# Kernel optimization log

Measured on AMD Instinct MI355X. Metric: run time of the kernel, lower is better.

The kernel has to match this reference:

```python
import jax, jax.numpy as jnp
import numpy as np

BATCH = 4096
DIM = 256
TEMP = 0.5
COS_EPS = 1e-8  # torch.nn.CosineSimilarity default eps


def setup_inputs() -> dict:
    key = jax.random.key(0)
    k1, k2 = jax.random.split(key)
    zis = jax.random.normal(k1, (BATCH, DIM), dtype=jnp.float32)
    zjs = jax.random.normal(k2, (BATCH, DIM), dtype=jnp.float32)
    return {"zis": zis, "zjs": zjs}


def reference(zis, zjs):
    n = zis.shape[0]  # batch_size
    # representations = cat([zjs, zis]) -> (2N, D)
    reps = jnp.concatenate([zjs, zis], axis=0)
    # cosine similarity matrix: dot / max(|x||y|, eps)  (matches torch CosineSimilarity)
    norms = jnp.linalg.norm(reps, axis=-1)  # (2N,)
    sim = (reps @ reps.T) / jnp.maximum(norms[:, None] * norms[None, :], COS_EPS)  # (2N, 2N)
    # positives: diag at offset +N (rows 0..N-1) then offset -N (rows N..2N-1)
    pos = jnp.concatenate([jnp.diagonal(sim, n), jnp.diagonal(sim, -n)])  # (2N,)
    # CE with label 0 over [pos, negatives]: negatives = row minus {diag, positive};
    # logsumexp([pos] + negatives) == logsumexp(row with only the self-diagonal masked),
    # since the positive appears exactly once in the row.
    two_n = 2 * n
    logits = sim / TEMP
    logits = jnp.where(jnp.eye(two_n, dtype=bool), -jnp.inf, logits)
    lse = jax.nn.logsumexp(logits, axis=-1)  # (2N,)
    loss = jnp.sum(lse - pos / TEMP)  # CrossEntropyLoss(reduction='sum')
    return loss / two_n
```

## Files before the change

kernel.cpp:

```cpp
#include <hip/hip_runtime.h>
#include <hip/hip_bf16.h>

#define TWO_N  8192
#define N_HALF 4096
#define DIMS   256

typedef float f32x4 __attribute__((ext_vector_type(4)));

__device__ __forceinline__ float fast_exp2(float x) {
#if __has_builtin(__builtin_amdgcn_exp2f)
    return __builtin_amdgcn_exp2f(x);
#else
    float r; asm("v_exp_f32 %0, %1" : "=v"(r) : "v"(x)); return r;
#endif
}

#define GLOAD_LDS16(g, l)                                                      \
    __builtin_amdgcn_global_load_lds(                                          \
        (const __attribute__((address_space(1))) unsigned int*)(g),            \
        (__attribute__((address_space(3))) unsigned int*)(l), 16, 0, 0)

__global__ __launch_bounds__(256) void nrm_kernel(const float* __restrict__ zis,
                                                  const float* __restrict__ zjs,
                                                  unsigned char* __restrict__ swz,
                                                  float* __restrict__ out)
{
    if (blockIdx.x == 0 && threadIdx.x == 0) out[0] = 0.f;

    const int tid = threadIdx.x;
    const int l32 = tid & 31;
    const int row = blockIdx.x * 8 + (tid >> 5);
    const int k0  = l32 * 8;

    const float* src = (row < N_HALF) ? (zjs + (size_t)row * DIMS)
                                      : (zis + (size_t)(row - N_HALF) * DIMS);
    const float4 v0 = reinterpret_cast<const float4*>(src + k0)[0];
    const float4 v1 = reinterpret_cast<const float4*>(src + k0 + 4)[0];
    float ss = v0.x * v0.x + v0.y * v0.y + v0.z * v0.z + v0.w * v0.w
             + v1.x * v1.x + v1.y * v1.y + v1.z * v1.z + v1.w * v1.w;
#pragma unroll
    for (int m = 1; m < 32; m <<= 1) ss += __shfl_xor(ss, m, 64);
    const float inv = rsqrtf(ss) * 1.69864360045f;

    int w0 = 0, w1 = 0;
    w0 = __builtin_amdgcn_cvt_pk_fp8_f32(v0.x * inv, v0.y * inv, w0, 0);
    w0 = __builtin_amdgcn_cvt_pk_fp8_f32(v0.z * inv, v0.w * inv, w0, 1);
    w1 = __builtin_amdgcn_cvt_pk_fp8_f32(v1.x * inv, v1.y * inv, w1, 0);
    w1 = __builtin_amdgcn_cvt_pk_fp8_f32(v1.z * inv, v1.w * inv, w1, 1);

    const size_t byte = ((size_t)((row >> 4) * 8 + (l32 >> 2)) * 64
                         + (l32 & 3) * 16 + (row & 15)) * 8;
    int2 o; o.x = w0; o.y = w1;
    *reinterpret_cast<int2*>(swz + byte) = o;
}

__global__ __launch_bounds__(512, 4) void ntx_kernel(const unsigned char* __restrict__ swz,
                                                     float* __restrict__ rowsum_part,
                                                     float* __restrict__ pos_part)
{
    __shared__ unsigned char abuf[2][16384];

    const int lane = threadIdx.x & 63;
    const int wave = threadIdx.x >> 6;
    const int l15  = lane & 15;
    const int quad = lane >> 4;

    const int rg   = blockIdx.x & 15;
    const int cs   = blockIdx.x >> 4;
    const int wr0  = rg * 512 + wave * 64;
    const int p0   = wr0 ^ N_HALF;

    auto stage = [&](int buf, int c) {
        const unsigned char* gsrc = swz + ((size_t)(cs * 128 + c * 32)) * 512
                                  + wave * 2048 + lane * 16;
        GLOAD_LDS16(gsrc,       &abuf[buf][wave * 2048]);
        GLOAD_LDS16(gsrc + 1024, &abuf[buf][wave * 2048 + 1024]);
    };

    stage(0, 0);

    long long bfrag[4][8];
#pragma unroll
    for (int t = 0; t < 4; ++t) {
        const unsigned char* bp = swz + (size_t)((wr0 >> 4) + t) * 4096 + lane * 8;
#pragma unroll
        for (int kk = 0; kk < 8; ++kk)
            bfrag[t][kk] = *reinterpret_cast<const long long*>(bp + kk * 512);
    }

    float sum_exp[4] = {0.f, 0.f, 0.f, 0.f};
    float pos_acc = 0.f;

    asm volatile("s_waitcnt vmcnt(0)" ::: "memory");
    __syncthreads();

    int cur = 0;
    for (int c = 0; c < 4; ++c) {
        if (c < 3) stage(cur ^ 1, c + 1);

        const int cc_base = cs * 256 + c * 64;

#pragma unroll
        for (int it = 0; it < 4; ++it) {
            const unsigned char* ab = &abuf[cur][it * 4096 + lane * 8];

            f32x4 acc[4] = {{0.f, 0.f, 0.f, 0.f}, {0.f, 0.f, 0.f, 0.f},
                            {0.f, 0.f, 0.f, 0.f}, {0.f, 0.f, 0.f, 0.f}};
#pragma unroll
            for (int h = 0; h < 2; ++h) {
                long long a[4];
#pragma unroll
                for (int k4 = 0; k4 < 4; ++k4)
                    a[k4] = *reinterpret_cast<const long long*>(ab + (h * 4 + k4) * 512);
#pragma unroll
                for (int k4 = 0; k4 < 4; ++k4) {
#pragma unroll
                    for (int t = 0; t < 4; ++t)
                        acc[t] = __builtin_amdgcn_mfma_f32_16x16x32_fp8_fp8(
                            a[k4], bfrag[t][h * 4 + k4], acc[t], 0, 0, 0);
                }
            }

            const int c0 = cc_base + it * 16;
            const bool special = (c0 < wr0 + 64 && c0 + 16 > wr0) ||
                                 (c0 < p0 + 64 && c0 + 16 > p0);
            if (!special) {
#pragma unroll
                for (int t = 0; t < 4; ++t)
#pragma unroll
                    for (int j = 0; j < 4; ++j)
                        sum_exp[t] += fast_exp2(acc[t][j]);
            } else {
#pragma unroll
                for (int t = 0; t < 4; ++t) {
                    const int r = wr0 + t * 16 + l15;
#pragma unroll
                    for (int j = 0; j < 4; ++j) {
                        const int col = c0 + quad * 4 + j;
                        const float e = fast_exp2(acc[t][j]);
                        sum_exp[t] += (col == r) ? 0.f : e;
                        if (col == (r ^ N_HALF)) pos_acc += acc[t][j];
                    }
                }
            }
        }

        asm volatile("s_waitcnt vmcnt(0)" ::: "memory");
        __syncthreads();
        cur ^= 1;
    }

#pragma unroll
    for (int t = 0; t < 4; ++t) {
        float s = sum_exp[t];
        s += __shfl_xor(s, 16, 64);
        s += __shfl_xor(s, 32, 64);
        if (lane < 16)
            rowsum_part[(size_t)cs * TWO_N + wr0 + t * 16 + lane] = s;
    }

#pragma unroll
    for (int m = 1; m < 64; m <<= 1) pos_acc += __shfl_xor(pos_acc, m, 64);
    if (lane == 0) pos_part[blockIdx.x * 8 + wave] = pos_acc;
}

__global__ __launch_bounds__(1024) void fin1_kernel(const float* __restrict__ rowsum_part,
                                                    const float* __restrict__ pos_part,
                                                    float* __restrict__ out)
{
    __shared__ float red[16];
    const int t = threadIdx.x;
    const int r = blockIdx.x * 1024 + t;
    float acc = 0.f;
#pragma unroll
    for (int cs = 0; cs < 32; ++cs)
        acc += rowsum_part[(size_t)cs * TWO_N + r];
    float v = logf(acc);
    if (r < 4096)
        v -= 0.69314718055994531f * pos_part[r];
#pragma unroll
    for (int m = 1; m < 64; m <<= 1) v += __shfl_xor(v, m, 64);
    if ((t & 63) == 0) red[t >> 6] = v;
    __syncthreads();
    if (t == 0) {
        float s = 0.f;
#pragma unroll
        for (int w = 0; w < 16; ++w) s += red[w];
        atomicAdd(out, s / (float)TWO_N);
    }
}

extern "C" void kernel_launch(void* const* d_in, const int* in_sizes, int n_in,
                              void* d_out, int out_size, void* d_ws, size_t ws_size,
                              hipStream_t stream)
{
    const float* zis = (const float*)d_in[0];
    const float* zjs = (const float*)d_in[1];

    unsigned char* swz = (unsigned char*)d_ws;
    float* rowsum_part = (float*)((char*)d_ws + (size_t)TWO_N * DIMS);
    float* pos_part    = rowsum_part + (size_t)32 * TWO_N;

    nrm_kernel<<<TWO_N / 8, 256, 0, stream>>>(zis, zjs, swz, (float*)d_out);
    ntx_kernel<<<512, 512, 0, stream>>>(swz, rowsum_part, pos_part);
    fin1_kernel<<<8, 1024, 0, stream>>>(rowsum_part, pos_part, (float*)d_out);
}
```

Before: 87.56 us.

## Switch fp8 MFMA to 16x16x128 scaled MX instruction with new swizzle layout

Replaces the sixteen 16x16x32 fp8 MFMAs per tile with two 16x16x128 scaled fp8 MFMAs (unit scales, 0x7F), which issue fewer instructions per K step. The normalized fp8 buffer is re-swizzled so each lane holds 32 contiguous K bytes, matching the operand layout of the wider instruction. Fragments are now loaded as 32-byte vectors from LDS and global memory. The risks are LDS bank conflicts from the new 32-byte stride and incorrect results if the scale or layout encoding is wrong.

```diff
diff --git a/kernel.cpp b/kernel.cpp
--- a/kernel.cpp
+++ b/kernel.cpp
@@ -6,6 +6,7 @@
 #define DIMS   256
 
 typedef float f32x4 __attribute__((ext_vector_type(4)));
+typedef int   i32x8 __attribute__((ext_vector_type(8)));
 
 __device__ __forceinline__ float fast_exp2(float x) {
 #if __has_builtin(__builtin_amdgcn_exp2f)
@@ -15,6 +16,13 @@
 #endif
 }
 
+__device__ __forceinline__ f32x4 mfma_mx(i32x8 a, i32x8 b, f32x4 c) {
+    return __builtin_amdgcn_mfma_scale_f32_16x16x128_f8f6f4(
+        a, b, c, 0 , 0 ,
+        0 , 0x7F ,
+        0 , 0x7F );
+}
+
 #define GLOAD_LDS16(g, l)                                                      \
     __builtin_amdgcn_global_load_lds(                                          \
         (const __attribute__((address_space(1))) unsigned int*)(g),            \
@@ -48,8 +56,8 @@
     w1 = __builtin_amdgcn_cvt_pk_fp8_f32(v1.x * inv, v1.y * inv, w1, 0);
     w1 = __builtin_amdgcn_cvt_pk_fp8_f32(v1.z * inv, v1.w * inv, w1, 1);
 
-    const size_t byte = ((size_t)((row >> 4) * 8 + (l32 >> 2)) * 64
-                         + (l32 & 3) * 16 + (row & 15)) * 8;
+    const size_t byte = (size_t)((row >> 4) * 2 + (l32 >> 4)) * 2048
+                      + (size_t)((l32 >> 2) & 3) * 512 + (row & 15) * 32 + (l32 & 3) * 8;
     int2 o; o.x = w0; o.y = w1;
     *reinterpret_cast<int2*>(swz + byte) = o;
 }
@@ -71,21 +79,21 @@
     const int p0   = wr0 ^ N_HALF;
 
     auto stage = [&](int buf, int c) {
-        const unsigned char* gsrc = swz + ((size_t)(cs * 128 + c * 32)) * 512
+        const unsigned char* gsrc = swz + (size_t)cs * 65536 + (size_t)c * 16384
                                   + wave * 2048 + lane * 16;
-        GLOAD_LDS16(gsrc,       &abuf[buf][wave * 2048]);
+        GLOAD_LDS16(gsrc,        &abuf[buf][wave * 2048]);
         GLOAD_LDS16(gsrc + 1024, &abuf[buf][wave * 2048 + 1024]);
     };
 
     stage(0, 0);
 
-    long long bfrag[4][8];
+    i32x8 bfrag[4][2];
 #pragma unroll
     for (int t = 0; t < 4; ++t) {
-        const unsigned char* bp = swz + (size_t)((wr0 >> 4) + t) * 4096 + lane * 8;
-#pragma unroll
-        for (int kk = 0; kk < 8; ++kk)
-            bfrag[t][kk] = *reinterpret_cast<const long long*>(bp + kk * 512);
+        const unsigned char* bp = swz + (size_t)(((wr0 >> 4) + t) * 2) * 2048
+                                + quad * 512 + l15 * 32;
+        bfrag[t][0] = *reinterpret_cast<const i32x8*>(bp);
+        bfrag[t][1] = *reinterpret_cast<const i32x8*>(bp + 2048);
     }
 
     float sum_exp[4] = {0.f, 0.f, 0.f, 0.f};
@@ -102,24 +110,18 @@
 
 #pragma unroll
         for (int it = 0; it < 4; ++it) {
-            const unsigned char* ab = &abuf[cur][it * 4096 + lane * 8];
+            const unsigned char* ab = &abuf[cur][it * 4096 + quad * 512 + l15 * 32];
+            const i32x8 a0 = *reinterpret_cast<const i32x8*>(ab);
+            const i32x8 a1 = *reinterpret_cast<const i32x8*>(ab + 2048);
 
             f32x4 acc[4] = {{0.f, 0.f, 0.f, 0.f}, {0.f, 0.f, 0.f, 0.f},
                             {0.f, 0.f, 0.f, 0.f}, {0.f, 0.f, 0.f, 0.f}};
 #pragma unroll
-            for (int h = 0; h < 2; ++h) {
-                long long a[4];
-#pragma unroll
-                for (int k4 = 0; k4 < 4; ++k4)
-                    a[k4] = *reinterpret_cast<const long long*>(ab + (h * 4 + k4) * 512);
-#pragma unroll
-                for (int k4 = 0; k4 < 4; ++k4) {
-#pragma unroll
-                    for (int t = 0; t < 4; ++t)
-                        acc[t] = __builtin_amdgcn_mfma_f32_16x16x32_fp8_fp8(
-                            a[k4], bfrag[t][h * 4 + k4], acc[t], 0, 0, 0);
-                }
-            }
+            for (int t = 0; t < 4; ++t)
+                acc[t] = mfma_mx(a0, bfrag[t][0], acc[t]);
+#pragma unroll
+            for (int t = 0; t < 4; ++t)
+                acc[t] = mfma_mx(a1, bfrag[t][1], acc[t]);
 
             const int c0 = cc_base + it * 16;
             const bool special = (c0 < wr0 + 64 && c0 + 16 > wr0) ||
```

Result: slower. 95.21 us (+8.7%).
